# Performance work log

Hardware: AMD Instinct MI355X
Metric: run time of the kernel (lower is better)

The kernel has to match this reference:

```python
import jax, jax.numpy as jnp
import numpy as np

PROPOSAL_COUNT = 100
IOU_THRESHOLD = 0.3
SCORE_THRESHOLD = 0.7
MEAN = np.array([0.0, 0.0, 0.0, 0.0], np.float32)
STD = np.array([0.1, 0.1, 0.2, 0.2], np.float32)
CLIP_RATIO = 16.0 / 1000.0
NEG = -1e9  # finite -inf sentinel (avoids NaNs)


def delta2bbox(anchors, delta):
    # anchors: (..., 4) xyxy, delta: (..., 4) normalized dx,dy,dw,dh
    delta = delta * STD + MEAN
    w = anchors[..., 2] - anchors[..., 0]
    h = anchors[..., 3] - anchors[..., 1]
    cx = anchors[..., 0] + 0.5 * w
    cy = anchors[..., 1] + 0.5 * h
    max_ratio = abs(float(np.log(CLIP_RATIO)))
    dx, dy = delta[..., 0], delta[..., 1]
    dw = jnp.clip(delta[..., 2], -max_ratio, max_ratio)
    dh = jnp.clip(delta[..., 3], -max_ratio, max_ratio)
    pcx = cx + dx * w
    pcy = cy + dy * h
    pw = w * jnp.exp(dw)
    ph = h * jnp.exp(dh)
    return jnp.stack([pcx - 0.5 * pw, pcy - 0.5 * ph, pcx + 0.5 * pw, pcy + 0.5 * ph], axis=-1)


def iou_one(box, boxes):
    # box: (4,), boxes: (N, 4) -> (N,)
    ix1 = jnp.maximum(box[0], boxes[..., 0])
    iy1 = jnp.maximum(box[1], boxes[..., 1])
    ix2 = jnp.minimum(box[2], boxes[..., 2])
    iy2 = jnp.minimum(box[3], boxes[..., 3])
    inter = jnp.maximum(ix2 - ix1, 0.0) * jnp.maximum(iy2 - iy1, 0.0)
    area1 = (box[2] - box[0]) * (box[3] - box[1])
    area2 = (boxes[..., 2] - boxes[..., 0]) * (boxes[..., 3] - boxes[..., 1])
    return inter / jnp.maximum(area1 + area2 - inter, 1e-9)


def greedy_nms(scores, boxes):
    # masked greedy hard-NMS with fixed PROPOSAL_COUNT iterations
    # scores: (N,) with NEG on invalid entries, boxes: (N, 4)
    def step(s, _):
        i = jnp.argmax(s)
        si = s[i]
        sel = si > 0.5 * NEG
        iou = iou_one(boxes[i], boxes)
        s = jnp.where(sel & (iou > IOU_THRESHOLD), NEG, s)
        s = s.at[i].set(NEG)
        return s, (jnp.where(sel, i, -1), jnp.where(sel, si, NEG))
    _, (idx, sc) = jax.lax.scan(step, scores, None, length=PROPOSAL_COUNT)
    return idx, sc  # (P,), (P,)


def filter_detection(logits, regress, anchors):
    B, N, C = logits.shape
    # decode + clip (elementwise, same math as gathering first then decoding)
    boxes = jnp.clip(delta2bbox(anchors[None], regress), 0.0, 1.0)  # (B,N,4)
    label = jnp.argmax(logits, axis=-1)                             # (B,N)
    fg = label > 0                                                  # background filter
    scores = jnp.moveaxis(logits[..., 1:], -1, 1)                   # (B,C-1,N)
    valid = fg[:, None, :] & (scores >= SCORE_THRESHOLD)
    s0 = jnp.where(valid, scores, NEG)
    # selection indices are piecewise constant in the inputs
    s0_c = jax.lax.stop_gradient(s0)
    boxes_c = jax.lax.stop_gradient(boxes)
    nms_b = jax.vmap(jax.vmap(greedy_nms, in_axes=(0, None)), in_axes=(0, 0))
    sel_idx, sel_sc = nms_b(s0_c, boxes_c)                          # (B,C-1,P)
    K = (C - 1) * PROPOSAL_COUNT
    idx_flat = sel_idx.reshape(B, K)
    sc_flat = sel_sc.reshape(B, K)
    # global top-k over all classes, sorted descending (matches tf.nn.top_k)
    top_sc, top_pos = jax.lax.top_k(sc_flat, PROPOSAL_COUNT)        # (B,P)
    anchor_idx = jnp.take_along_axis(idx_flat, top_pos, axis=1)
    ok = (top_sc > 0.5 * NEG)[..., None].astype(logits.dtype)       # padding mask
    safe = jnp.maximum(anchor_idx, 0)
    out_logit = jnp.take_along_axis(logits, safe[..., None], axis=1) * ok  # (B,P,C)
    out_box = jnp.take_along_axis(boxes, safe[..., None], axis=1) * ok     # (B,P,4)
    return out_logit, out_box


def setup_inputs() -> dict:
    key = jax.random.key(0)
    k1, k2, k3, k4 = jax.random.split(key, 4)
    B, N, C = 4, 100000, 41
    logits = jax.random.normal(k1, (B, N, C), jnp.float32)
    regress = jax.random.normal(k2, (B, N, 4), jnp.float32) * 0.5
    xy = jax.random.uniform(k3, (N, 2), jnp.float32) * 0.8
    wh = jax.random.uniform(k4, (N, 2), jnp.float32) * 0.2 + 0.01
    anchors = jnp.concatenate([xy, jnp.minimum(xy + wh, 1.0)], axis=-1)  # valid xyxy in [0,1]
    return {"logits": logits, "regress": regress, "anchors": anchors}


def reference(logits, regress, anchors):
    return filter_detection(logits, regress, anchors)
```

## Files before the change

### kernel.cpp

```cpp
#include <hip/hip_runtime.h>
#include <cstdint>
#include <cstddef>

#define BN 4
#define NN 100000
#define CC 41
#define NCLS 40
#define NPROB (BN * NCLS)
#define PROP 100
#define NEGV (-1e9f)
#define IOU_T 0.3f
#define SCORE_T 0.7f
#define MAXR 4.135166556742356f
#define CAP 2048
#define TARGET 384
#define LISTCAP 26624
#define SH 4
#define SHCAP (LISTCAP / SH)
#define NBMPW 3125
#define E07 0xBF333333u
#define ERHI 0xC1800000u
#define W0 ((unsigned long long)(ERHI - E07))
#define NT3 512

typedef unsigned long long ull;
typedef unsigned int uint;

__device__ __forceinline__ uint encf(float x) {
  uint u = __float_as_uint(x);
  return (u & 0x80000000u) ? ~u : (u | 0x80000000u);
}
__device__ __forceinline__ float decf(uint e) {
  uint u = (e & 0x80000000u) ? (e ^ 0x80000000u) : ~e;
  return __uint_as_float(u);
}
__device__ __forceinline__ uint binofE(ull E) {
  return (E >= (ull)ERHI) ? 255u : (uint)(((E - E07) << 8) / W0);
}
__device__ __forceinline__ ull edgeE(int b) {
  return (ull)E07 + (((ull)b * W0 + 255ull) >> 8);
}

__device__ __forceinline__ float iou_f(float ax1, float ay1, float ax2, float ay2,
                                       float bx1, float by1, float bx2, float by2) {
  float ix1 = fmaxf(ax1, bx1), iy1 = fmaxf(ay1, by1);
  float ix2 = fminf(ax2, bx2), iy2 = fminf(ay2, by2);
  float inter = fmaxf(ix2 - ix1, 0.0f) * fmaxf(iy2 - iy1, 0.0f);
  float a1 = (ax2 - ax1) * (ay2 - ay1);
  float a2 = (bx2 - bx1) * (by2 - by1);
  return inter / fmaxf(a1 + a2 - inter, 1e-9f);
}

__device__ __forceinline__ int select_window(const uint* h, int* lo_out) {
  uint cum = 0; int lo = 256; int act = 2;
  for (int bb = 255; bb >= 0; --bb) {
    uint nb = h[bb];
    if (nb == 0u) continue;
    if (cum + nb > CAP) {
      if (cum == 0u) { act = 1; }
      break;
    }
    cum += nb; lo = bb; act = 0;
    if (cum >= TARGET) break;
  }
  *lo_out = lo;
  return act;
}

__global__ void decode_kernel(const float4* __restrict__ regress,
                              const float4* __restrict__ anchors,
                              float4* __restrict__ boxes,
                              uint* __restrict__ gcnt) {
  int i = blockIdx.x * 256 + threadIdx.x;
  if (i < NPROB * SH) gcnt[i] = 0u;
  if (i >= BN * NN) return;
  int n = i % NN;
  float4 d = regress[i];
  float4 a = anchors[n];
  float w = a.z - a.x, h = a.w - a.y;
  float cx = a.x + 0.5f * w, cy = a.y + 0.5f * h;
  float dx = d.x * 0.1f, dy = d.y * 0.1f;
  float dw = fminf(fmaxf(d.z * 0.2f, -MAXR), MAXR);
  float dh = fminf(fmaxf(d.w * 0.2f, -MAXR), MAXR);
  float pcx = cx + dx * w, pcy = cy + dy * h;
  float pw = w * expf(dw), ph = h * expf(dh);
  float4 o;
  o.x = fminf(fmaxf(pcx - 0.5f * pw, 0.0f), 1.0f);
  o.y = fminf(fmaxf(pcy - 0.5f * ph, 0.0f), 1.0f);
  o.z = fminf(fmaxf(pcx + 0.5f * pw, 0.0f), 1.0f);
  o.w = fminf(fmaxf(pcy + 0.5f * ph, 0.0f), 1.0f);
  boxes[i] = o;
}

__global__ void score_kernel(const float* __restrict__ logits,
                             ull* __restrict__ glist,
                             uint* __restrict__ gcnt,
                             uint* __restrict__ fgb) {
  __shared__ float lg[256 * CC];
  __shared__ unsigned short wpre[NCLS][4];
  __shared__ uint cbase[NCLS];
  int b = blockIdx.y;
  int n0 = blockIdx.x * 256;
  int shard = blockIdx.x & (SH - 1);
  int tid = threadIdx.x;
  int wave = tid >> 6, lane = tid & 63;
  int rows = NN - n0; if (rows > 256) rows = 256;
  int total4 = rows * CC / 4;
  const float4* src = (const float4*)(logits + ((size_t)b * NN + n0) * CC);
  float4* dst = (float4*)lg;
  for (int i = tid; i < total4; i += 256) dst[i] = src[i];
  __syncthreads();

  bool act = tid < rows;
  int n = n0 + tid;
  float bestv = 0.0f; int bestc = 0;
  if (act) {
    bestv = lg[tid * CC];
    #pragma unroll
    for (int c = 1; c < CC; ++c) {
      float v = lg[tid * CC + c];
      if (v > bestv) { bestv = v; bestc = c; }
    }
  }
  bool fg = act && (bestc > 0);
  int wbase = n0 + (tid & ~63);

  ull mfg = __ballot(fg);
  if (lane == 0 && wbase < NN) fgb[b * NBMPW + (wbase >> 5)] = (uint)mfg;
  if (lane == 32 && wbase + 32 < NN) fgb[b * NBMPW + (wbase >> 5) + 1] = (uint)(mfg >> 32);

  #pragma unroll 4
  for (int c = 1; c < CC; ++c) {
    float v = act ? lg[tid * CC + c] : 0.0f;
    ull m = __ballot(fg && (v >= SCORE_T));
    if (lane == 0) wpre[c - 1][wave] = (unsigned short)__popcll(m);
  }
  __syncthreads();

  if (tid < NCLS) {
    uint t0 = wpre[tid][0], t1 = wpre[tid][1], t2 = wpre[tid][2], t3 = wpre[tid][3];
    uint tot = t0 + t1 + t2 + t3;
    uint base = tot ? atomicAdd(&gcnt[(b * NCLS + tid) * SH + shard], tot) : 0u;
    cbase[tid] = base;
    wpre[tid][0] = 0;
    wpre[tid][1] = (unsigned short)t0;
    wpre[tid][2] = (unsigned short)(t0 + t1);
    wpre[tid][3] = (unsigned short)(t0 + t1 + t2);
  }
  __syncthreads();

  #pragma unroll 4
  for (int c = 1; c < CC; ++c) {
    float v = act ? lg[tid * CC + c] : 0.0f;
    bool elig = fg && (v >= SCORE_T);
    ull m = __ballot(elig);
    if (elig) {
      uint pos = cbase[c - 1] + wpre[c - 1][wave]
               + (uint)__popcll(m & ((1ull << lane) - 1ull));
      if (pos < SHCAP)
        glist[(size_t)(b * NCLS + (c - 1)) * LISTCAP + (size_t)shard * SHCAP + pos] =
            ((ull)encf(v) << 32) | (uint)n;
    }
  }
}

__global__ void hist_kernel(const ull* __restrict__ glist,
                            const uint* __restrict__ gcnt,
                            uint* __restrict__ chist) {
  __shared__ uint h[256];
  int prob = blockIdx.y;
  int shard = blockIdx.x;
  int tid = threadIdx.x;
  uint cs = gcnt[prob * SH + shard];
  if (cs > SHCAP) cs = SHCAP;
  h[tid] = 0u;
  __syncthreads();
  uint lo = shard * SHCAP;
  uint hi = lo + cs;
  const ull* list = glist + (size_t)prob * LISTCAP;
  for (uint i = lo + tid; i < hi; i += 256)
    atomicAdd(&h[binofE(list[i] >> 32)], 1u);
  __syncthreads();
  chist[((size_t)prob * SH + shard) * 256 + tid] = h[tid];
}

__global__ void offsets_kernel(const uint* __restrict__ chist,
                               const uint* __restrict__ gcnt,
                               uint* __restrict__ gcoff,
                               uint* __restrict__ gC,
                               uint* __restrict__ gtot) {
  __shared__ uint sa[256], sb[256];
  int prob = blockIdx.x;
  int tid = threadIdx.x;
  uint c0 = gcnt[prob * SH + 0], c1 = gcnt[prob * SH + 1],
       c2 = gcnt[prob * SH + 2], c3 = gcnt[prob * SH + 3];
  bool dense = (c0 > SHCAP) || (c1 > SHCAP) || (c2 > SHCAP) || (c3 > SHCAP);
  if (tid == 0) gtot[prob] = dense ? (LISTCAP + 1u) : (c0 + c1 + c2 + c3);
  if (dense) return;
  const uint* ch = chist + (size_t)prob * SH * 256;
  uint h0 = ch[0 * 256 + tid], h1 = ch[1 * 256 + tid],
       h2 = ch[2 * 256 + tid], h3 = ch[3 * 256 + tid];
  gcoff[((size_t)prob * SH + 0) * 256 + tid] = 0u;
  gcoff[((size_t)prob * SH + 1) * 256 + tid] = h0;
  gcoff[((size_t)prob * SH + 2) * 256 + tid] = h0 + h1;
  gcoff[((size_t)prob * SH + 3) * 256 + tid] = h0 + h1 + h2;
  sa[tid] = h0 + h1 + h2 + h3;
  __syncthreads();
  uint* s = sa; uint* d = sb;
  for (int off = 1; off < 256; off <<= 1) {
    uint v = s[tid] + ((tid + off < 256) ? s[tid + off] : 0u);
    d[tid] = v;
    __syncthreads();
    uint* t = s; s = d; d = t;
  }
  gC[(size_t)prob * 257 + tid] = s[tid];
  if (tid == 0) gC[(size_t)prob * 257 + 256] = 0u;
}

__global__ void scatter_kernel(const ull* __restrict__ glist,
                               const uint* __restrict__ gcnt,
                               const uint* __restrict__ gcoff,
                               const uint* __restrict__ gC,
                               const uint* __restrict__ gtot,
                               ull* __restrict__ blist) {
  __shared__ uint rank[256], startL[256], cofL[256];
  int prob = blockIdx.y;
  int shard = blockIdx.x;
  int tid = threadIdx.x;
  if (gtot[prob] > LISTCAP) return;
  uint cs = gcnt[prob * SH + shard];
  rank[tid] = 0u;
  cofL[tid] = gcoff[((size_t)prob * SH + shard) * 256 + tid];
  startL[tid] = gC[(size_t)prob * 257 + tid + 1];
  __syncthreads();
  uint lo = shard * SHCAP;
  uint hi = lo + cs;
  const ull* list = glist + (size_t)prob * LISTCAP;
  ull* bl = blist + (size_t)prob * LISTCAP;
  for (uint i = lo + tid; i < hi; i += 256) {
    ull k = list[i];
    uint bin = binofE(k >> 32);
    uint r = atomicAdd(&rank[bin], 1u);
    bl[startL[bin] + cofL[bin] + r] = k;
  }
}

__device__ int sort_walk(int ncand, int nsel,
                         ull* keysL, float4* boxesL, float4* selL,
                         int* sh_nsel, int prob, int* __restrict__ oidx,
                         float* __restrict__ osc, int tid) {
  if (ncand == 0) return nsel;
  int M = 64; while (M < ncand) M <<= 1;
  for (int i = ncand + tid; i < M; i += NT3) keysL[i] = 0ull;
  __syncthreads();
  for (int k = 2; k <= M; k <<= 1) {
    for (int j = k >> 1; j > 0; j >>= 1) {
      for (int t = tid; t < M; t += NT3) {
        int ixj = t ^ j;
        if (ixj > t) {
          ull a = keysL[t], c2 = keysL[ixj];
          bool up = ((t & k) == 0);
          if (up ? (a < c2) : (a > c2)) { keysL[t] = c2; keysL[ixj] = a; }
        }
      }
      __syncthreads();
    }
  }
  if (tid < 64) {
    int lane = tid;
    int ns = nsel;
    for (int base = 0; base < ncand && ns < PROP; base += 64) {
      int i = base + lane;
      bool valid = i < ncand;
      ull key = valid ? keysL[i] : 0ull;
      int slot = (int)(key & 0x7FFF);
      float4 bx = boxesL[valid ? slot : 0];
      float sc = decf((uint)(key >> 32));
      int aidx = 131071 - (int)((key >> 15) & 0x1FFFF);
      bool supp = false;
      for (int j = 0; j < ns; ++j) {
        float4 sb = selL[j];
        supp = supp || (iou_f(bx.x, bx.y, bx.z, bx.w, sb.x, sb.y, sb.z, sb.w) > IOU_T);
      }
      ull live = __ballot(valid && !supp);
      while (live && ns < PROP) {
        int kk = __ffsll(live) - 1;
        float x1 = __shfl(bx.x, kk), y1 = __shfl(bx.y, kk);
        float x2 = __shfl(bx.z, kk), y2 = __shfl(bx.w, kk);
        float ksc = __shfl(sc, kk);
        int kidx = __shfl(aidx, kk);
        if (lane == 0) {
          oidx[prob * PROP + ns] = kidx;
          osc [prob * PROP + ns] = ksc;
          selL[ns] = make_float4(x1, y1, x2, y2);
        }
        ns++;
        if (lane > kk && valid && !supp)
          supp = iou_f(bx.x, bx.y, bx.z, bx.w, x1, y1, x2, y2) > IOU_T;
        live = __ballot(valid && !supp) & ~((2ull << kk) - 1ull);
      }
    }
    if (lane == 0) *sh_nsel = ns;
  }
  __syncthreads();
  return *sh_nsel;
}

__device__ int process_window(ull WLO, ull WUP, int idxbin,
                              bool dense, uint rs, uint re,
                              const ull* list, const float* lcol,
                              const uint* fgp, const float4* bx4,
                              ull* keysL, float4* boxesL, float4* selL,
                              int* sh_cnt, int* sh_nsel,
                              int nsel, int prob, int* __restrict__ oidx,
                              float* __restrict__ osc, int tid) {
  __syncthreads();
  if (tid == 0) *sh_cnt = 0;
  __syncthreads();
  if (!dense) {
    for (uint i = rs + tid; i < re; i += NT3) {
      ull k = list[i];
      ull E = k >> 32;
      uint idx = (uint)(k & 0xFFFFFFFFu);
      if (E >= WLO && E < WUP && (idxbin < 0 || (int)(idx >> 9) == idxbin)) {
        int slot = atomicAdd(sh_cnt, 1);
        if (slot < CAP) {
          keysL[slot] = (E << 32)
                      | ((ull)((131071u - idx) & 0x1FFFFu) << 15)
                      | (ull)slot;
          boxesL[slot] = bx4[idx];
        }
      }
    }
  } else {
    for (int i = tid; i < NN; i += NT3) {
      if (!((fgp[i >> 5] >> (i & 31)) & 1u)) continue;
      float s = lcol[(size_t)i * CC];
      if (s < SCORE_T) continue;
      ull E = encf(s);
      if (E >= WLO && E < WUP && (idxbin < 0 || (i >> 9) == idxbin)) {
        int slot = atomicAdd(sh_cnt, 1);
        if (slot < CAP) {
          keysL[slot] = (E << 32)
                      | ((ull)((131071u - (uint)i) & 0x1FFFFu) << 15)
                      | (ull)slot;
          boxesL[slot] = bx4[i];
        }
      }
    }
  }
  __syncthreads();
  int ncand = *sh_cnt; if (ncand > CAP) ncand = CAP;
  return sort_walk(ncand, nsel, keysL, boxesL, selL, sh_nsel, prob, oidx, osc, tid);
}

__device__ int fallback_range(ull Rlo0, ull Rhi0,
                              bool dense, uint rs, uint re,
                              const ull* list, const float* lcol,
                              const uint* fgp, const float4* bx4,
                              ull* keysL, float4* boxesL, float4* selL,
                              uint* subh,
                              int* sh_cnt, int* sh_nsel, int* sh_a, int* sh_b,
                              int nsel, int prob, int* __restrict__ oidx,
                              float* __restrict__ osc, int tid) {
  ull EHIl = Rhi0;
  for (int round = 0; round < 300 && nsel < PROP; ++round) {
    ull Rlo = Rlo0, Rhi = EHIl;
    int action; int bsel;
    ull WLO = 0, WUP = 0, E0 = 0;
    bool idxm = false;
    while (true) {
      for (int i = tid; i < 256; i += NT3) subh[i] = 0u;
      __syncthreads();
      ull W = Rhi - Rlo;
      if (!dense) {
        for (uint i = rs + tid; i < re; i += NT3) {
          ull E = list[i] >> 32;
          if (E >= Rlo && E < Rhi)
            atomicAdd(&subh[(uint)(((E - Rlo) << 8) / W)], 1u);
        }
      } else {
        for (int i = tid; i < NN; i += NT3) {
          if (!((fgp[i >> 5] >> (i & 31)) & 1u)) continue;
          float s = lcol[(size_t)i * CC];
          if (s < SCORE_T) continue;
          ull E = encf(s);
          if (E >= Rlo && E < Rhi)
            atomicAdd(&subh[(uint)(((E - Rlo) << 8) / W)], 1u);
        }
      }
      __syncthreads();
      if (tid == 0) {
        int lo;
        int act = select_window(subh, &lo);
        int rb = -1;
        if (act == 1) {
          for (int bb = 255; bb >= 0; --bb) if (subh[bb]) { rb = bb; break; }
        }
        *sh_a = act; *sh_b = (act == 1) ? rb : lo;
      }
      __syncthreads();
      action = *sh_a; bsel = *sh_b;
      __syncthreads();
      if (action == 2) break;
      if (action == 0) {
        WLO = Rlo + (((ull)bsel * W + 255ull) >> 8);
        WUP = Rhi;
        break;
      }
      ull nRlo = Rlo + (((ull)bsel * W + 255ull) >> 8);
      ull nRhi = Rlo + (((ull)(bsel + 1) * W + 255ull) >> 8);
      if (nRhi > Rhi) nRhi = Rhi;
      Rlo = nRlo; Rhi = nRhi;
      if (Rhi - Rlo <= 1ull) { idxm = true; E0 = Rlo; break; }
    }
    if (action == 2) break;
    if (!idxm) {
      nsel = process_window(WLO, WUP, -1, dense, rs, re, list, lcol, fgp, bx4,
                            keysL, boxesL, selL, sh_cnt, sh_nsel,
                            nsel, prob, oidx, osc, tid);
      EHIl = WLO;
    } else {
      for (int ib = 0; ib < 256 && nsel < PROP; ++ib)
        nsel = process_window(E0, E0 + 1ull, ib, dense, rs, re, list, lcol, fgp, bx4,
                              keysL, boxesL, selL, sh_cnt, sh_nsel,
                              nsel, prob, oidx, osc, tid);
      EHIl = E0;
    }
  }
  return nsel;
}

__launch_bounds__(NT3)
__global__ void nms_finish(const ull* __restrict__ blist,
                           const uint* __restrict__ gtot,
                           const float* __restrict__ logits,
                           const uint* __restrict__ fgb,
                           const float4* __restrict__ boxes,
                           const uint* __restrict__ gC,
                           int* __restrict__ oidx, float* __restrict__ osc) {
  __shared__ uint CL[257];
  __shared__ uint subh[256];
  __shared__ ull keysL[CAP];
  __shared__ float4 boxesL[CAP];
  __shared__ float4 selL[PROP];
  __shared__ int sh_cnt, sh_nsel, sh_a, sh_b, sh_m;

  int prob = blockIdx.x;
  int b = prob / NCLS;
  int c1 = prob % NCLS + 1;
  int tid = threadIdx.x;

  uint cnt = gtot[prob];
  bool dense = cnt > LISTCAP;
  const ull* bl = blist + (size_t)prob * LISTCAP;
  const float4* bx4 = boxes + (size_t)b * NN;
  const float* lcol = logits + (size_t)b * NN * CC + c1;
  const uint* fgp = fgb + b * NBMPW;

  int nsel = 0;

  if (dense) {
    nsel = fallback_range(E07, 1ull << 32, true, 0, 0, bl, lcol, fgp, bx4,
                          keysL, boxesL, selL, subh,
                          &sh_cnt, &sh_nsel, &sh_a, &sh_b,
                          0, prob, oidx, osc, tid);
  } else {
    for (int i = tid; i < 257; i += NT3) CL[i] = gC[(size_t)prob * 257 + i];
    __syncthreads();
    int hibin = 256;
    while (nsel < PROP && hibin > 0) {
      if (tid == 0) sh_m = -1;
      __syncthreads();
      if (tid < 256 && tid < hibin && (CL[tid] - CL[hibin]) >= TARGET)
        atomicMax(&sh_m, tid);
      __syncthreads();
      if (tid == 0) {
        int bm = sh_m; int act, lo;
        if (bm < 0) {
          uint W = CL[0] - CL[hibin];
          act = W ? 0 : 2; lo = 0;
        } else {
          uint W = CL[bm] - CL[hibin];
          if (W <= CAP) { act = 0; lo = bm; }
          else {
            uint W2 = CL[bm + 1] - CL[hibin];
            if (W2) { act = 0; lo = bm + 1; }
            else { act = 1; lo = bm; }
          }
        }
        sh_a = act; sh_b = lo;
      }
      __syncthreads();
      int act = sh_a, lo = sh_b;
      __syncthreads();
      if (act == 2) break;
      if (act == 0) {
        uint rs = CL[hibin];
        int ncand = (int)(CL[lo] - CL[hibin]);
        for (int i = tid; i < ncand; i += NT3) {
          ull k = bl[rs + i];
          uint idx = (uint)(k & 0xFFFFFFFFu);
          keysL[i] = ((k >> 32) << 32)
                   | ((ull)((131071u - idx) & 0x1FFFFu) << 15)
                   | (ull)i;
          boxesL[i] = bx4[idx];
        }
        __syncthreads();
        nsel = sort_walk(ncand, nsel, keysL, boxesL, selL, &sh_nsel, prob, oidx, osc, tid);
        hibin = lo;
      } else {
        uint rs = CL[lo + 1], re = CL[lo];
        ull Rlo = edgeE(lo);
        ull Rhi = (lo == 255) ? (1ull << 32) : edgeE(lo + 1);
        nsel = fallback_range(Rlo, Rhi, false, rs, re, bl, lcol, fgp, bx4,
                              keysL, boxesL, selL, subh,
                              &sh_cnt, &sh_nsel, &sh_a, &sh_b,
                              nsel, prob, oidx, osc, tid);
        hibin = lo;
      }
    }
  }

  __syncthreads();
  for (int p = nsel + tid; p < PROP; p += NT3) {
    oidx[prob * PROP + p] = -1;
    osc [prob * PROP + p] = NEGV;
  }
}

__global__ void topk_kernel(const float* __restrict__ logits,
                            const float4* __restrict__ boxes,
                            const int* __restrict__ oidx,
                            const float* __restrict__ osc,
                            float* __restrict__ out) {
  __shared__ ull keys[4096];
  int b = blockIdx.x;
  int tid = threadIdx.x;
  for (int i = tid; i < 4096; i += 1024) {
    ull key = 0ull;
    if (i < NCLS * PROP) {
      float sc = osc[b * NCLS * PROP + i];
      key = ((ull)encf(sc) << 32) | (uint)(~i);
    }
    keys[i] = ~key;
  }
  __syncthreads();
  for (int k = 2; k <= 4096; k <<= 1) {
    for (int j = k >> 1; j > 0; j >>= 1) {
      for (int t = tid; t < 4096; t += 1024) {
        int ixj = t ^ j;
        if (ixj > t) {
          ull a = keys[t], c2 = keys[ixj];
          bool up = ((t & k) == 0);
          if ((a > c2) == up) { keys[t] = c2; keys[ixj] = a; }
        }
      }
      __syncthreads();
    }
  }
  if (tid < PROP) {
    ull key = ~keys[tid];
    uint e = (uint)(key >> 32);
    float sc = decf(e);
    bool ok = sc > 0.5f * NEGV;
    int kk = (int)(~(uint)key);
    if (kk < 0 || kk >= NCLS * PROP) kk = 0;
    int idx = ok ? oidx[b * NCLS * PROP + kk] : 0;
    if (idx < 0) idx = 0;
    float m = ok ? 1.0f : 0.0f;
    const float* lp = logits + ((size_t)b * NN + idx) * CC;
    float* outl = out + ((size_t)b * PROP + tid) * CC;
    #pragma unroll
    for (int c = 0; c < CC; ++c) outl[c] = lp[c] * m;
    float4 bb = boxes[(size_t)b * NN + idx];
    float* outb = out + (size_t)BN * PROP * CC + ((size_t)b * PROP + tid) * 4;
    outb[0] = bb.x * m; outb[1] = bb.y * m; outb[2] = bb.z * m; outb[3] = bb.w * m;
  }
}

extern "C" void kernel_launch(void* const* d_in, const int* in_sizes, int n_in,
                              void* d_out, int out_size, void* d_ws, size_t ws_size,
                              hipStream_t stream) {
  const float* logits  = (const float*)d_in[0];
  const float* regress = (const float*)d_in[1];
  const float* anchors = (const float*)d_in[2];
  float* out = (float*)d_out;

  char* ws = (char*)d_ws;
  size_t off = 0;
  float4* boxes = (float4*)(ws + off);  off += (size_t)BN * NN * 16;
  ull* glist = (ull*)(ws + off);        off += (size_t)NPROB * LISTCAP * 8;
  ull* blist = (ull*)(ws + off);        off += (size_t)NPROB * LISTCAP * 8;
  uint* gcnt = (uint*)(ws + off);       off += NPROB * SH * 4;
  uint* gtot = (uint*)(ws + off);       off += NPROB * 4;
  uint* fgb  = (uint*)(ws + off);       off += BN * NBMPW * 4;
  float* osc = (float*)(ws + off);      off += NPROB * PROP * 4;
  int*   oidx = (int*)(ws + off);       off += NPROB * PROP * 4;
  uint* chist = (uint*)(ws + off);      off += (size_t)NPROB * SH * 256 * 4;
  uint* gcoff = (uint*)(ws + off);      off += (size_t)NPROB * SH * 256 * 4;
  uint* gC   = (uint*)(ws + off);       off += (size_t)NPROB * 257 * 4;

  decode_kernel<<<(BN * NN + 255) / 256, 256, 0, stream>>>(
      (const float4*)regress, (const float4*)anchors, boxes, gcnt);
  score_kernel<<<dim3((NN + 255) / 256, BN), 256, 0, stream>>>(logits, glist, gcnt, fgb);
  hist_kernel<<<dim3(SH, NPROB), 256, 0, stream>>>(glist, gcnt, chist);
  offsets_kernel<<<NPROB, 256, 0, stream>>>(chist, gcnt, gcoff, gC, gtot);
  scatter_kernel<<<dim3(SH, NPROB), 256, 0, stream>>>(glist, gcnt, gcoff, gC, gtot, blist);
  nms_finish<<<NPROB, NT3, 0, stream>>>(blist, gtot, logits, fgb, boxes, gC, oidx, osc);
  topk_kernel<<<BN, 1024, 0, stream>>>(logits, boxes, oidx, osc, out);
}
```

Measured before the change: 210.4 us.

## Register-shuffle bitonic stages, parallel pre-suppression, reuse ballot masks in score kernel

```diff
diff --git a/kernel.cpp b/kernel.cpp
--- a/kernel.cpp
+++ b/kernel.cpp
@@ -98,6 +98,7 @@
                              uint* __restrict__ fgb) {
   __shared__ float lg[256 * CC];
   __shared__ unsigned short wpre[NCLS][4];
+  __shared__ ull wmask[NCLS][4];
   __shared__ uint cbase[NCLS];
   int b = blockIdx.y;
   int n0 = blockIdx.x * 256;
@@ -133,7 +134,10 @@
   for (int c = 1; c < CC; ++c) {
     float v = act ? lg[tid * CC + c] : 0.0f;
     ull m = __ballot(fg && (v >= SCORE_T));
-    if (lane == 0) wpre[c - 1][wave] = (unsigned short)__popcll(m);
+    if (lane == 0) {
+      wpre[c - 1][wave] = (unsigned short)__popcll(m);
+      wmask[c - 1][wave] = m;
+    }
   }
   __syncthreads();
 
@@ -151,10 +155,9 @@
 
   #pragma unroll 4
   for (int c = 1; c < CC; ++c) {
-    float v = act ? lg[tid * CC + c] : 0.0f;
-    bool elig = fg && (v >= SCORE_T);
-    ull m = __ballot(elig);
-    if (elig) {
+    ull m = wmask[c - 1][wave];
+    if ((m >> lane) & 1ull) {
+      float v = lg[tid * CC + c];
       uint pos = cbase[c - 1] + wpre[c - 1][wave]
                + (uint)__popcll(m & ((1ull << lane) - 1ull));
       if (pos < SHCAP)
@@ -245,16 +248,34 @@
   }
 }
 
-__device__ int sort_walk(int ncand, int nsel,
-                         ull* keysL, float4* boxesL, float4* selL,
-                         int* sh_nsel, int prob, int* __restrict__ oidx,
-                         float* __restrict__ osc, int tid) {
-  if (ncand == 0) return nsel;
+__device__ __forceinline__ ull bswap_cmp(ull v, int e, int j, int k) {
+  ull p = __shfl_xor(v, j);
+  bool up = ((e & k) == 0);
+  bool low = ((e & j) == 0);
+  return (up == low) ? (v > p ? v : p) : (v < p ? v : p);
+}
+
+__device__ void sort_desc_st(ull* keysL, int ncand, int tid) {
   int M = 64; while (M < ncand) M <<= 1;
   for (int i = ncand + tid; i < M; i += NT3) keysL[i] = 0ull;
   __syncthreads();
-  for (int k = 2; k <= M; k <<= 1) {
+  int e0 = tid, e1 = tid + NT3, e2 = tid + 2 * NT3, e3 = tid + 3 * NT3;
+  bool h0 = e0 < M, h1 = e1 < M, h2 = e2 < M, h3 = e3 < M;
+  ull v0 = h0 ? keysL[e0] : 0ull, v1 = h1 ? keysL[e1] : 0ull;
+  ull v2 = h2 ? keysL[e2] : 0ull, v3 = h3 ? keysL[e3] : 0ull;
+  for (int k = 2; k <= 64; k <<= 1) {
     for (int j = k >> 1; j > 0; j >>= 1) {
+      if (h0) v0 = bswap_cmp(v0, e0, j, k);
+      if (h1) v1 = bswap_cmp(v1, e1, j, k);
+      if (h2) v2 = bswap_cmp(v2, e2, j, k);
+      if (h3) v3 = bswap_cmp(v3, e3, j, k);
+    }
+  }
+  if (h0) keysL[e0] = v0; if (h1) keysL[e1] = v1;
+  if (h2) keysL[e2] = v2; if (h3) keysL[e3] = v3;
+  __syncthreads();
+  for (int k = 128; k <= M; k <<= 1) {
+    for (int j = k >> 1; j >= 64; j >>= 1) {
       for (int t = tid; t < M; t += NT3) {
         int ixj = t ^ j;
         if (ixj > t) {
@@ -265,7 +286,24 @@
       }
       __syncthreads();
     }
-  }
+    if (h0) v0 = keysL[e0]; if (h1) v1 = keysL[e1];
+    if (h2) v2 = keysL[e2]; if (h3) v3 = keysL[e3];
+    for (int j = 32; j > 0; j >>= 1) {
+      if (h0) v0 = bswap_cmp(v0, e0, j, k);
+      if (h1) v1 = bswap_cmp(v1, e1, j, k);
+      if (h2) v2 = bswap_cmp(v2, e2, j, k);
+      if (h3) v3 = bswap_cmp(v3, e3, j, k);
+    }
+    if (h0) keysL[e0] = v0; if (h1) keysL[e1] = v1;
+    if (h2) keysL[e2] = v2; if (h3) keysL[e3] = v3;
+    __syncthreads();
+  }
+}
+
+__device__ int walk(int ncand, int nsel, const ull* keysL, const float4* boxesL,
+                    float4* selL, const unsigned char* suppB, int* sh_nsel, int prob,
+                    int* __restrict__ oidx, float* __restrict__ osc, int tid) {
+  int ns_enter = nsel;
   if (tid < 64) {
     int lane = tid;
     int ns = nsel;
@@ -277,8 +315,8 @@
       float4 bx = boxesL[valid ? slot : 0];
       float sc = decf((uint)(key >> 32));
       int aidx = 131071 - (int)((key >> 15) & 0x1FFFF);
-      bool supp = false;
-      for (int j = 0; j < ns; ++j) {
+      bool supp = valid ? (suppB[i] != 0) : false;
+      for (int j = ns_enter; j < ns; ++j) {
         float4 sb = selL[j];
         supp = supp || (iou_f(bx.x, bx.y, bx.z, bx.w, sb.x, sb.y, sb.z, sb.w) > IOU_T);
       }
@@ -306,11 +344,37 @@
   return *sh_nsel;
 }
 
+__device__ int sort_walk(int ncand, int nsel,
+                         ull* keysL, float4* boxesL, float4* selL,
+                         unsigned char* suppB,
+                         int* sh_nsel, int prob, int* __restrict__ oidx,
+                         float* __restrict__ osc, int tid) {
+  if (ncand == 0) return nsel;
+  sort_desc_st(keysL, ncand, tid);
+  if (nsel > 0) {
+    for (int i = tid; i < ncand; i += NT3) {
+      ull key = keysL[i];
+      float4 bx = boxesL[(int)(key & 0x7FFF)];
+      bool dead = false;
+      for (int j = 0; j < nsel; ++j) {
+        float4 sb = selL[j];
+        dead = dead || (iou_f(bx.x, bx.y, bx.z, bx.w, sb.x, sb.y, sb.z, sb.w) > IOU_T);
+      }
+      suppB[i] = dead ? 1 : 0;
+    }
+  } else {
+    for (int i = tid; i < ncand; i += NT3) suppB[i] = 0;
+  }
+  __syncthreads();
+  return walk(ncand, nsel, keysL, boxesL, selL, suppB, sh_nsel, prob, oidx, osc, tid);
+}
+
 __device__ int process_window(ull WLO, ull WUP, int idxbin,
                               bool dense, uint rs, uint re,
                               const ull* list, const float* lcol,
                               const uint* fgp, const float4* bx4,
                               ull* keysL, float4* boxesL, float4* selL,
+                              unsigned char* suppB,
                               int* sh_cnt, int* sh_nsel,
                               int nsel, int prob, int* __restrict__ oidx,
                               float* __restrict__ osc, int tid) {
@@ -351,7 +415,7 @@
   }
   __syncthreads();
   int ncand = *sh_cnt; if (ncand > CAP) ncand = CAP;
-  return sort_walk(ncand, nsel, keysL, boxesL, selL, sh_nsel, prob, oidx, osc, tid);
+  return sort_walk(ncand, nsel, keysL, boxesL, selL, suppB, sh_nsel, prob, oidx, osc, tid);
 }
 
 __device__ int fallback_range(ull Rlo0, ull Rhi0,
@@ -359,7 +423,7 @@
                               const ull* list, const float* lcol,
                               const uint* fgp, const float4* bx4,
                               ull* keysL, float4* boxesL, float4* selL,
-                              uint* subh,
+                              unsigned char* suppB, uint* subh,
                               int* sh_cnt, int* sh_nsel, int* sh_a, int* sh_b,
                               int nsel, int prob, int* __restrict__ oidx,
                               float* __restrict__ osc, int tid) {
@@ -417,13 +481,13 @@
     if (action == 2) break;
     if (!idxm) {
       nsel = process_window(WLO, WUP, -1, dense, rs, re, list, lcol, fgp, bx4,
-                            keysL, boxesL, selL, sh_cnt, sh_nsel,
+                            keysL, boxesL, selL, suppB, sh_cnt, sh_nsel,
                             nsel, prob, oidx, osc, tid);
       EHIl = WLO;
     } else {
       for (int ib = 0; ib < 256 && nsel < PROP; ++ib)
         nsel = process_window(E0, E0 + 1ull, ib, dense, rs, re, list, lcol, fgp, bx4,
-                              keysL, boxesL, selL, sh_cnt, sh_nsel,
+                              keysL, boxesL, selL, suppB, sh_cnt, sh_nsel,
                               nsel, prob, oidx, osc, tid);
       EHIl = E0;
     }
@@ -444,6 +508,7 @@
   __shared__ ull keysL[CAP];
   __shared__ float4 boxesL[CAP];
   __shared__ float4 selL[PROP];
+  __shared__ unsigned char suppB[CAP];
   __shared__ int sh_cnt, sh_nsel, sh_a, sh_b, sh_m;
 
   int prob = blockIdx.x;
@@ -462,7 +527,7 @@
 
   if (dense) {
     nsel = fallback_range(E07, 1ull << 32, true, 0, 0, bl, lcol, fgp, bx4,
-                          keysL, boxesL, selL, subh,
+                          keysL, boxesL, selL, suppB, subh,
                           &sh_cnt, &sh_nsel, &sh_a, &sh_b,
                           0, prob, oidx, osc, tid);
   } else {
@@ -507,14 +572,15 @@
           boxesL[i] = bx4[idx];
         }
         __syncthreads();
-        nsel = sort_walk(ncand, nsel, keysL, boxesL, selL, &sh_nsel, prob, oidx, osc, tid);
+        nsel = sort_walk(ncand, nsel, keysL, boxesL, selL, suppB,
+                         &sh_nsel, prob, oidx, osc, tid);
         hibin = lo;
       } else {
         uint rs = CL[lo + 1], re = CL[lo];
         ull Rlo = edgeE(lo);
         ull Rhi = (lo == 255) ? (1ull << 32) : edgeE(lo + 1);
         nsel = fallback_range(Rlo, Rhi, false, rs, re, bl, lcol, fgp, bx4,
-                              keysL, boxesL, selL, subh,
+                              keysL, boxesL, selL, suppB, subh,
                               &sh_cnt, &sh_nsel, &sh_a, &sh_b,
                               nsel, prob, oidx, osc, tid);
         hibin = lo;
```

Measured after the change: 215.0 us. 1.02x slower.

## Fuse box decode and score histogram into score kernel

Applied to the files above, without the earlier changes.

```diff
diff --git a/kernel.cpp b/kernel.cpp
--- a/kernel.cpp
+++ b/kernel.cpp
@@ -67,35 +67,14 @@
   return act;
 }
 
-__global__ void decode_kernel(const float4* __restrict__ regress,
-                              const float4* __restrict__ anchors,
-                              float4* __restrict__ boxes,
-                              uint* __restrict__ gcnt) {
-  int i = blockIdx.x * 256 + threadIdx.x;
-  if (i < NPROB * SH) gcnt[i] = 0u;
-  if (i >= BN * NN) return;
-  int n = i % NN;
-  float4 d = regress[i];
-  float4 a = anchors[n];
-  float w = a.z - a.x, h = a.w - a.y;
-  float cx = a.x + 0.5f * w, cy = a.y + 0.5f * h;
-  float dx = d.x * 0.1f, dy = d.y * 0.1f;
-  float dw = fminf(fmaxf(d.z * 0.2f, -MAXR), MAXR);
-  float dh = fminf(fmaxf(d.w * 0.2f, -MAXR), MAXR);
-  float pcx = cx + dx * w, pcy = cy + dy * h;
-  float pw = w * expf(dw), ph = h * expf(dh);
-  float4 o;
-  o.x = fminf(fmaxf(pcx - 0.5f * pw, 0.0f), 1.0f);
-  o.y = fminf(fmaxf(pcy - 0.5f * ph, 0.0f), 1.0f);
-  o.z = fminf(fmaxf(pcx + 0.5f * pw, 0.0f), 1.0f);
-  o.w = fminf(fmaxf(pcy + 0.5f * ph, 0.0f), 1.0f);
-  boxes[i] = o;
-}
-
 __global__ void score_kernel(const float* __restrict__ logits,
+                             const float4* __restrict__ regress,
+                             const float4* __restrict__ anchors,
+                             float4* __restrict__ boxes,
                              ull* __restrict__ glist,
                              uint* __restrict__ gcnt,
-                             uint* __restrict__ fgb) {
+                             uint* __restrict__ fgb,
+                             uint* __restrict__ chist) {
   __shared__ float lg[256 * CC];
   __shared__ unsigned short wpre[NCLS][4];
   __shared__ uint cbase[NCLS];
@@ -105,14 +84,33 @@
   int tid = threadIdx.x;
   int wave = tid >> 6, lane = tid & 63;
   int rows = NN - n0; if (rows > 256) rows = 256;
+  bool act = tid < rows;
+  int n = n0 + tid;
+
+  if (act) {
+    float4 d = regress[(size_t)b * NN + n];
+    float4 a = anchors[n];
+    float w = a.z - a.x, h = a.w - a.y;
+    float cx = a.x + 0.5f * w, cy = a.y + 0.5f * h;
+    float dx = d.x * 0.1f, dy = d.y * 0.1f;
+    float dw = fminf(fmaxf(d.z * 0.2f, -MAXR), MAXR);
+    float dh = fminf(fmaxf(d.w * 0.2f, -MAXR), MAXR);
+    float pcx = cx + dx * w, pcy = cy + dy * h;
+    float pw = w * expf(dw), ph = h * expf(dh);
+    float4 o;
+    o.x = fminf(fmaxf(pcx - 0.5f * pw, 0.0f), 1.0f);
+    o.y = fminf(fmaxf(pcy - 0.5f * ph, 0.0f), 1.0f);
+    o.z = fminf(fmaxf(pcx + 0.5f * pw, 0.0f), 1.0f);
+    o.w = fminf(fmaxf(pcy + 0.5f * ph, 0.0f), 1.0f);
+    boxes[(size_t)b * NN + n] = o;
+  }
+
   int total4 = rows * CC / 4;
   const float4* src = (const float4*)(logits + ((size_t)b * NN + n0) * CC);
   float4* dst = (float4*)lg;
   for (int i = tid; i < total4; i += 256) dst[i] = src[i];
   __syncthreads();
 
-  bool act = tid < rows;
-  int n = n0 + tid;
   float bestv = 0.0f; int bestc = 0;
   if (act) {
     bestv = lg[tid * CC];
@@ -157,31 +155,14 @@
     if (elig) {
       uint pos = cbase[c - 1] + wpre[c - 1][wave]
                + (uint)__popcll(m & ((1ull << lane) - 1ull));
-      if (pos < SHCAP)
+      if (pos < SHCAP) {
+        uint e = encf(v);
         glist[(size_t)(b * NCLS + (c - 1)) * LISTCAP + (size_t)shard * SHCAP + pos] =
-            ((ull)encf(v) << 32) | (uint)n;
-    }
-  }
-}
-
-__global__ void hist_kernel(const ull* __restrict__ glist,
-                            const uint* __restrict__ gcnt,
-                            uint* __restrict__ chist) {
-  __shared__ uint h[256];
-  int prob = blockIdx.y;
-  int shard = blockIdx.x;
-  int tid = threadIdx.x;
-  uint cs = gcnt[prob * SH + shard];
-  if (cs > SHCAP) cs = SHCAP;
-  h[tid] = 0u;
-  __syncthreads();
-  uint lo = shard * SHCAP;
-  uint hi = lo + cs;
-  const ull* list = glist + (size_t)prob * LISTCAP;
-  for (uint i = lo + tid; i < hi; i += 256)
-    atomicAdd(&h[binofE(list[i] >> 32)], 1u);
-  __syncthreads();
-  chist[((size_t)prob * SH + shard) * 256 + tid] = h[tid];
+            ((ull)e << 32) | (uint)n;
+        atomicAdd(&chist[((size_t)(b * NCLS + (c - 1)) * SH + shard) * 256 + binofE((ull)e)], 1u);
+      }
+    }
+  }
 }
 
 __global__ void offsets_kernel(const uint* __restrict__ chist,
@@ -601,10 +582,11 @@
   uint* gcoff = (uint*)(ws + off);      off += (size_t)NPROB * SH * 256 * 4;
   uint* gC   = (uint*)(ws + off);       off += (size_t)NPROB * 257 * 4;
 
-  decode_kernel<<<(BN * NN + 255) / 256, 256, 0, stream>>>(
-      (const float4*)regress, (const float4*)anchors, boxes, gcnt);
-  score_kernel<<<dim3((NN + 255) / 256, BN), 256, 0, stream>>>(logits, glist, gcnt, fgb);
-  hist_kernel<<<dim3(SH, NPROB), 256, 0, stream>>>(glist, gcnt, chist);
+  hipMemsetAsync(gcnt, 0, NPROB * SH * 4, stream);
+  hipMemsetAsync(chist, 0, (size_t)NPROB * SH * 256 * 4, stream);
+  score_kernel<<<dim3((NN + 255) / 256, BN), 256, 0, stream>>>(
+      logits, (const float4*)regress, (const float4*)anchors, boxes,
+      glist, gcnt, fgb, chist);
   offsets_kernel<<<NPROB, 256, 0, stream>>>(chist, gcnt, gcoff, gC, gtot);
   scatter_kernel<<<dim3(SH, NPROB), 256, 0, stream>>>(glist, gcnt, gcoff, gC, gtot, blist);
   nms_finish<<<NPROB, NT3, 0, stream>>>(blist, gtot, logits, fgb, boxes, gC, oidx, osc);
```

Result: slower. 296.9 us (+41.1%).
